# Optimization experiments

Hardware: AMD Instinct MI355X
Metric: run time of the kernel (lower is better)

The kernel has to match this reference:

```python
import jax, jax.numpy as jnp
import numpy as np

NUM_EXPERTS = 8
TOP_K = 2


def setup_inputs() -> dict:
    key = jax.random.key(0)
    ks = jax.random.split(key, 6)
    d, h, E = 512, 2048, NUM_EXPERTS
    s = 0.02
    return {
        "x": jax.random.normal(ks[0], (4, 4096, d), dtype=jnp.float32),
        "Wr": jax.random.normal(ks[1], (d, E), dtype=jnp.float32) * s,
        "W1": jax.random.normal(ks[2], (E, d, h), dtype=jnp.float32) * s,
        "b1": jax.random.normal(ks[3], (E, h), dtype=jnp.float32) * s,
        "W2": jax.random.normal(ks[4], (E, h, d), dtype=jnp.float32) * s,
        "b2": jax.random.normal(ks[5], (E, d), dtype=jnp.float32) * s,
    }


def reference(x, Wr, W1, b1, W2, b2):
    B, S, D = x.shape
    E = Wr.shape[1]
    flat = x.reshape(B * S, D)                      # [N, D]
    logits = flat @ Wr                              # [N, E]
    top_vals, top_idx = jax.lax.top_k(logits, TOP_K)  # [N, K]
    top_w = jax.nn.softmax(top_vals, axis=-1)       # [N, K]
    N = flat.shape[0]
    # dense gate matrix: weight per (token, expert); zero for unselected experts
    gates = jnp.zeros((N, E), dtype=flat.dtype).at[
        jnp.arange(N)[:, None], top_idx
    ].add(top_w)                                    # [N, E]
    out = jnp.zeros_like(flat)
    for e in range(E):  # small fixed expert count
        hdn = jax.nn.gelu(flat @ W1[e] + b1[e], approximate=False)  # [N, H]
        y = hdn @ W2[e] + b2[e]                                     # [N, D]
        out = out + gates[:, e:e + 1] * y
    return out.reshape(B, S, D)
```

## Files before the change

kernel.cpp:

```cpp
#include <hip/hip_runtime.h>
#include <math.h>

#define D_DIM 512
#define H_DIM 2048
#define NEXP  8

typedef __bf16 bf16x8 __attribute__((ext_vector_type(8)));
typedef float  f32x4  __attribute__((ext_vector_type(4)));

__device__ __forceinline__ unsigned short f2b(float f) {
    unsigned int u = __float_as_uint(f);
    unsigned int r = (u + 0x7FFFu + ((u >> 16) & 1u)) >> 16;
    return (unsigned short)r;
}

__device__ __forceinline__ float gelu_f(float v) {
    float z = fabsf(v) * 0.70710678118654752440f;
    float t = __builtin_amdgcn_rcpf(fmaf(0.3275911f, z, 1.0f));
    float poly = t * (0.254829592f +
                 t * (-0.284496736f +
                 t * (1.421413741f +
                 t * (-1.453152027f +
                 t * 1.061405429f))));
    float er = 1.0f - poly * __expf(-z * z);
    er = (v < 0.0f) ? -er : er;
    return 0.5f * v * (1.0f + er);
}

__device__ __forceinline__ void async_cp16(const void* g, void* l) {
    __builtin_amdgcn_global_load_lds(
        (const __attribute__((address_space(1))) unsigned int*)g,
        (__attribute__((address_space(3))) unsigned int*)l, 16, 0, 0);
}

__global__ void convert_x_kernel(const float* __restrict__ in,
                                 unsigned short* __restrict__ out, int n8) {
    int i = blockIdx.x * blockDim.x + threadIdx.x;
    if (i >= n8) return;
    const float4* p = (const float4*)(in + (size_t)i * 8);
    float4 a = p[0], b = p[1];
    unsigned short r[8] = {f2b(a.x), f2b(a.y), f2b(a.z), f2b(a.w),
                           f2b(b.x), f2b(b.y), f2b(b.z), f2b(b.w)};
    *(uint4*)(out + (size_t)i * 8) = *(const uint4*)r;
}

__global__ void transpose_conv_kernel(const float* __restrict__ in,
                                      unsigned short* __restrict__ out,
                                      int R, int C) {
    __shared__ unsigned short tile[64][72];
    int e = blockIdx.z;
    const float* ine = in + (size_t)e * R * C;
    unsigned short* oute = out + (size_t)e * C * R;
    int r0 = blockIdx.y * 64, c0 = blockIdx.x * 64;
    int tid = threadIdx.x;
#pragma unroll
    for (int rd = 0; rd < 4; ++rd) {
        int r = (tid >> 4) + rd * 16;
        int c = (tid & 15) * 4;
        float4 v = *(const float4*)&ine[(size_t)(r0 + r) * C + c0 + c];
        tile[c + 0][r] = f2b(v.x);
        tile[c + 1][r] = f2b(v.y);
        tile[c + 2][r] = f2b(v.z);
        tile[c + 3][r] = f2b(v.w);
    }
    __syncthreads();
    int cc = tid >> 2, rc = (tid & 3) * 16;
    unsigned short* op = oute + (size_t)(c0 + cc) * R + r0 + rc;
    *(uint4*)(op)     = *(const uint4*)&tile[cc][rc];
    *(uint4*)(op + 8) = *(const uint4*)&tile[cc][rc + 8];
}

__global__ void router_kernel(const float* __restrict__ x,
                              const float* __restrict__ Wr,
                              float* __restrict__ gate_w,
                              int* __restrict__ route,
                              int ntok) {
    int wid  = (blockIdx.x * blockDim.x + threadIdx.x) >> 6;
    int lane = threadIdx.x & 63;
    if (wid >= ntok) return;
    const float* xr = x + (size_t)wid * D_DIM;
    float acc[NEXP];
#pragma unroll
    for (int e = 0; e < NEXP; ++e) acc[e] = 0.0f;
#pragma unroll
    for (int it = 0; it < D_DIM / 64; ++it) {
        int d = it * 64 + lane;
        float xv = xr[d];
        const float* wr = Wr + d * NEXP;
#pragma unroll
        for (int e = 0; e < NEXP; ++e) acc[e] = fmaf(xv, wr[e], acc[e]);
    }
#pragma unroll
    for (int off = 32; off >= 1; off >>= 1) {
#pragma unroll
        for (int e = 0; e < NEXP; ++e) acc[e] += __shfl_xor(acc[e], off);
    }
    if (lane == 0) {
        int i0 = 0;
#pragma unroll
        for (int e = 1; e < NEXP; ++e) if (acc[e] > acc[i0]) i0 = e;
        int i1 = (i0 == 0) ? 1 : 0;
#pragma unroll
        for (int e = 0; e < NEXP; ++e) {
            if (e != i0 && acc[e] > acc[i1]) i1 = e;
        }
        float v0 = acc[i0], v1 = acc[i1];
        float ee = expf(v1 - v0);
        float inv = 1.0f / (1.0f + ee);
        int t = wid;
        gate_w[2 * t]     = inv;
        gate_w[2 * t + 1] = ee * inv;
        route[t] = i0 | (i1 << 8);
    }
}

__global__ void lists_kernel(const int* __restrict__ route,
                             int* __restrict__ lists,
                             int* __restrict__ cb,
                             int ntok) {
    __shared__ int wave_off[4];
    int e = blockIdx.x;
    int tid = threadIdx.x;
    int lane = tid & 63, w = tid >> 6;
    int running = 0;
    for (int c0 = 0; c0 < ntok; c0 += 256) {
        int t = c0 + tid;
        int rt = (t < ntok) ? route[t] : -1;
        int e0 = rt & 255, e1 = (rt >> 8) & 255;
        bool p1 = (e1 == e) && (rt >= 0);
        bool p  = ((e0 == e) && (rt >= 0)) || p1;
        unsigned long long mask = __ballot(p);
        int mypos = __popcll(mask & ((1ull << lane) - 1ull));
        int wcnt  = __popcll(mask);
        if (lane == 0) wave_off[w] = wcnt;
        __syncthreads();
        int wbase = 0;
#pragma unroll
        for (int i = 0; i < 4; ++i) if (i < w) wbase += wave_off[i];
        int total = wave_off[0] + wave_off[1] + wave_off[2] + wave_off[3];
        if (p) lists[(size_t)e * ntok + running + wbase + mypos] = 2 * t + (p1 ? 1 : 0);
        running += total;
        __syncthreads();
    }
    if (tid == 0) cb[e] = running;
}

__global__ void prefix_kernel(int* cb) {
    if (threadIdx.x == 0 && blockIdx.x == 0) {
        int s = 0;
#pragma unroll
        for (int e = 0; e < NEXP; ++e) { cb[8 + e] = s; s += cb[e]; }
    }
}

__global__ void bias_gate_kernel(const int* __restrict__ route,
                                 const float* __restrict__ gate_w,
                                 const float* __restrict__ b2,
                                 float* __restrict__ out, int ntok) {
    int t = blockIdx.x * 4 + (threadIdx.x >> 6);
    int lane = threadIdx.x & 63;
    if (t >= ntok) return;
    int rt = route[t];
    int e0 = rt & 255, e1 = (rt >> 8) & 255;
    float w0 = gate_w[2 * t], w1 = gate_w[2 * t + 1];
    const float4* p0 = (const float4*)(b2 + (size_t)e0 * D_DIM);
    const float4* p1 = (const float4*)(b2 + (size_t)e1 * D_DIM);
    float4* po = (float4*)(out + (size_t)t * D_DIM);
#pragma unroll
    for (int j = 0; j < 2; ++j) {
        float4 a = p0[lane * 2 + j], b = p1[lane * 2 + j];
        float4 r;
        r.x = w0 * a.x + w1 * b.x;
        r.y = w0 * a.y + w1 * b.y;
        r.z = w0 * a.z + w1 * b.z;
        r.w = w0 * a.w + w1 * b.w;
        po[lane * 2 + j] = r;
    }
}


__global__ __launch_bounds__(256, 2) void gemm1_kernel(
        const unsigned short* __restrict__ xb,
        const unsigned short* __restrict__ W1T,
        const float* __restrict__ b1,
        const float* __restrict__ gate_w,
        const int* __restrict__ lists,
        const int* __restrict__ cb,
        unsigned short* __restrict__ hdn,
        int ntok) {
    int bid = blockIdx.x;
    int e = bid & 7;
    int rest = bid >> 3;
    int ntile = rest & 15;
    int mt = rest >> 4;
    int cnt = cb[e];
    if (mt * 128 >= cnt) return;
    int base = cb[8 + e];

    __shared__ unsigned short As[2][8192];
    __shared__ unsigned short Bs[2][8192];
    __shared__ int   toksS[128];
    __shared__ float twS[128];

    int tid = threadIdx.x;
    int l = tid & 63, w = tid >> 6;
    int wm = (w & 1) * 64, wn = (w >> 1) * 64;

    if (tid < 128) {
        int idx = mt * 128 + tid;
        int entry = (idx < cnt) ? lists[(size_t)e * ntok + idx] : -1;
        toksS[tid] = (entry >= 0) ? (entry >> 1) : 0;
        twS[tid]   = (entry >= 0) ? gate_w[entry] : 0.0f;
    }
    __syncthreads();

    const char* Aglob[4];
    const char* Bglob[4];
    {
        int swz = ((l & 7) ^ (l >> 3)) * 16;
        const char* W1e = (const char*)(W1T + (size_t)e * H_DIM * D_DIM);
#pragma unroll
        for (int c = 0; c < 4; ++c) {
            int row = (w * 4 + c) * 8 + (l >> 3);
            Aglob[c] = (const char*)xb + (size_t)toksS[row] * 1024 + swz;
            Bglob[c] = W1e + (size_t)(ntile * 128 + row) * 1024 + swz;
        }
    }

    f32x4 acc[4][4];
#pragma unroll
    for (int i = 0; i < 4; ++i)
#pragma unroll
        for (int j = 0; j < 4; ++j) acc[i][j] = (f32x4){0.f, 0.f, 0.f, 0.f};

#pragma unroll
    for (int c = 0; c < 4; ++c) {
        async_cp16(Aglob[c], (char*)&As[0][0] + (w * 4 + c) * 1024);
        async_cp16(Bglob[c], (char*)&Bs[0][0] + (w * 4 + c) * 1024);
    }
    __syncthreads();

    for (int kc = 0; kc < 8; ++kc) {
        int cur = kc & 1;
        if (kc + 1 < 8) {
            int ko = (kc + 1) * 128;
#pragma unroll
            for (int c = 0; c < 4; ++c) {
                async_cp16(Aglob[c] + ko, (char*)&As[cur ^ 1][0] + (w * 4 + c) * 1024);
                async_cp16(Bglob[c] + ko, (char*)&Bs[cur ^ 1][0] + (w * 4 + c) * 1024);
            }
        }
        const char* Ab = (const char*)&As[cur][0];
        const char* Bb = (const char*)&Bs[cur][0];
#pragma unroll
        for (int ks = 0; ks < 2; ++ks) {
            int g = ks * 4 + (l >> 4);
            bf16x8 av[4], bv[4];
#pragma unroll
            for (int mf = 0; mf < 4; ++mf) {
                int m = wm + mf * 16 + (l & 15);
                av[mf] = *(const bf16x8*)(Ab + m * 128 + ((g ^ (m & 7)) * 16));
            }
#pragma unroll
            for (int nf = 0; nf < 4; ++nf) {
                int n = wn + nf * 16 + (l & 15);
                bv[nf] = *(const bf16x8*)(Bb + n * 128 + ((g ^ (n & 7)) * 16));
            }
#pragma unroll
            for (int mf = 0; mf < 4; ++mf)
#pragma unroll
                for (int nf = 0; nf < 4; ++nf)
                    acc[mf][nf] = __builtin_amdgcn_mfma_f32_16x16x32_bf16(
                        av[mf], bv[nf], acc[mf][nf], 0, 0, 0);
        }
        __syncthreads();
    }

    float twr[4][4];
#pragma unroll
    for (int mf = 0; mf < 4; ++mf)
#pragma unroll
        for (int r = 0; r < 4; ++r)
            twr[mf][r] = twS[wm + mf * 16 + (l >> 4) * 4 + r];
    const float* b1e = b1 + (size_t)e * H_DIM + ntile * 128;
    float b1v[4];
#pragma unroll
    for (int nf = 0; nf < 4; ++nf)
        b1v[nf] = b1e[wn + nf * 16 + (l & 15)];

    char* Lo = (char*)&As[0][0];
#pragma unroll
    for (int mf = 0; mf < 4; ++mf) {
#pragma unroll
        for (int nf = 0; nf < 4; ++nf) {
#pragma unroll
            for (int r = 0; r < 4; ++r) {
                int row = wm + mf * 16 + (l >> 4) * 4 + r;
                int col = wn + nf * 16 + (l & 15);
                float hv = twr[mf][r] * gelu_f(acc[mf][nf][r] + b1v[nf]);
                int byte = row * 256 + ((col * 2) ^ (((row >> 2) & 3) << 5));
                *(unsigned short*)(Lo + byte) = f2b(hv);
            }
        }
    }
    __syncthreads();
#pragma unroll
    for (int j = 0; j < 8; ++j) {
        int row = j * 16 + (tid >> 4);
        int c16 = tid & 15;
        uint4 v = *(const uint4*)(Lo + row * 256 + c16 * 16);
        int colchunk = c16 ^ (((row >> 2) & 3) << 1);
        int gr = mt * 128 + row;
        if (gr < cnt)
            *(uint4*)(hdn + (size_t)(base + gr) * H_DIM + ntile * 128 + colchunk * 8) = v;
    }
}

__global__ __launch_bounds__(256, 2) void gemm2_kernel(
        const unsigned short* __restrict__ hdn,
        const unsigned short* __restrict__ W2T,
        const int* __restrict__ lists,
        const int* __restrict__ cb,
        float* __restrict__ out,
        int ntok) {
    int bid = blockIdx.x;
    int e = bid & 7;
    int rest = bid >> 3;
    int ntile = rest & 3;
    int mt = rest >> 2;
    int cnt = cb[e];
    if (mt * 128 >= cnt) return;
    int base = cb[8 + e];

    __shared__ unsigned short As[2][8192];
    __shared__ unsigned short Bs[2][8192];
    __shared__ int toksS[128];

    int tid = threadIdx.x;
    int l = tid & 63, w = tid >> 6;
    int wm = (w & 1) * 64, wn = (w >> 1) * 64;

    if (tid < 128) {
        int idx = mt * 128 + tid;
        int entry = (idx < cnt) ? lists[(size_t)e * ntok + idx] : -1;
        toksS[tid] = (entry >= 0) ? (entry >> 1) : 0;
    }
    __syncthreads();

    const char* Aglob[4];
    const char* Bglob[4];
    {
        int swz = ((l & 7) ^ (l >> 3)) * 16;
        const char* W2e = (const char*)(W2T + (size_t)e * D_DIM * H_DIM);
#pragma unroll
        for (int c = 0; c < 4; ++c) {
            int row = (w * 4 + c) * 8 + (l >> 3);
            Aglob[c] = (const char*)hdn + (size_t)(base + mt * 128 + row) * 4096 + swz;
            Bglob[c] = W2e + (size_t)(ntile * 128 + row) * 4096 + swz;
        }
    }

    f32x4 acc[4][4];
#pragma unroll
    for (int i = 0; i < 4; ++i)
#pragma unroll
        for (int j = 0; j < 4; ++j) acc[i][j] = (f32x4){0.f, 0.f, 0.f, 0.f};

#pragma unroll
    for (int c = 0; c < 4; ++c) {
        async_cp16(Aglob[c], (char*)&As[0][0] + (w * 4 + c) * 1024);
        async_cp16(Bglob[c], (char*)&Bs[0][0] + (w * 4 + c) * 1024);
    }
    __syncthreads();

    for (int kc = 0; kc < 32; ++kc) {
        int cur = kc & 1;
        if (kc + 1 < 32) {
            int ko = (kc + 1) * 128;
#pragma unroll
            for (int c = 0; c < 4; ++c) {
                async_cp16(Aglob[c] + ko, (char*)&As[cur ^ 1][0] + (w * 4 + c) * 1024);
                async_cp16(Bglob[c] + ko, (char*)&Bs[cur ^ 1][0] + (w * 4 + c) * 1024);
            }
        }
        const char* Ab = (const char*)&As[cur][0];
        const char* Bb = (const char*)&Bs[cur][0];
#pragma unroll
        for (int ks = 0; ks < 2; ++ks) {
            int g = ks * 4 + (l >> 4);
            bf16x8 av[4], bv[4];
#pragma unroll
            for (int mf = 0; mf < 4; ++mf) {
                int m = wm + mf * 16 + (l & 15);
                av[mf] = *(const bf16x8*)(Ab + m * 128 + ((g ^ (m & 7)) * 16));
            }
#pragma unroll
            for (int nf = 0; nf < 4; ++nf) {
                int n = wn + nf * 16 + (l & 15);
                bv[nf] = *(const bf16x8*)(Bb + n * 128 + ((g ^ (n & 7)) * 16));
            }
#pragma unroll
            for (int mf = 0; mf < 4; ++mf)
#pragma unroll
                for (int nf = 0; nf < 4; ++nf)
                    acc[mf][nf] = __builtin_amdgcn_mfma_f32_16x16x32_bf16(
                        av[mf], bv[nf], acc[mf][nf], 0, 0, 0);
        }
        __syncthreads();
    }

#pragma unroll
    for (int mf = 0; mf < 4; ++mf) {
#pragma unroll
        for (int r = 0; r < 4; ++r) {
            int rl = wm + mf * 16 + (l >> 4) * 4 + r;
            int gr = mt * 128 + rl;
            if (gr < cnt) {
                float* op = out + (size_t)toksS[rl] * D_DIM + ntile * 128 + wn;
#pragma unroll
                for (int nf = 0; nf < 4; ++nf)
                    atomicAdd(op + nf * 16 + (l & 15), acc[mf][nf][r]);
            }
        }
    }
}

#define FBT 64
#define FKC 64
#define FHC 64
#define FTPB 512

__global__ __launch_bounds__(FTPB) void moe_fused_fallback(
        const float* __restrict__ x,
        const float* __restrict__ W1, const float* __restrict__ b1,
        const float* __restrict__ W2, const float* __restrict__ b2,
        const float* __restrict__ gate_w,
        const int* __restrict__ lists, const int* __restrict__ counts,
        float* __restrict__ out, int ntok, int tiles) {
    __shared__ __align__(16) float ldsA[FBT][FKC + 4];
    __shared__ __align__(16) float ldsB[FKC][FHC + 4];
    __shared__ int   toks[FBT];
    __shared__ float tw[FBT];
    int e = blockIdx.x / tiles;
    int tile = blockIdx.x % tiles;
    int cnt = counts[e];
    if (tile * FBT >= cnt) return;
    int tid = threadIdx.x;
    int srow = tid >> 3, scol = (tid & 7) * 8;
    int tg2 = tid >> 4, sg4 = tid & 15;
    if (tid < FBT) {
        int idx = tile * FBT + tid;
        int entry = (idx < cnt) ? lists[(size_t)e * ntok + idx] : -1;
        toks[tid] = (entry >= 0) ? (entry >> 1) : 0;
        tw[tid]   = (entry >= 0) ? gate_w[entry] : 0.0f;
    }
    __syncthreads();
    float yacc[2][32];
#pragma unroll
    for (int p = 0; p < 2; ++p)
#pragma unroll
        for (int i = 0; i < 32; ++i) yacc[p][i] = 0.0f;
    const float* W1e = W1 + (size_t)e * D_DIM * H_DIM;
    const float* W2e = W2 + (size_t)e * H_DIM * D_DIM;
    const float* b1e = b1 + (size_t)e * H_DIM;
    int t0 = tg2, t1 = tg2 + 32;
    for (int hc = 0; hc < H_DIM / FHC; ++hc) {
        float pre[2][4];
#pragma unroll
        for (int p = 0; p < 2; ++p)
#pragma unroll
            for (int j = 0; j < 4; ++j) pre[p][j] = 0.0f;
        for (int kc = 0; kc < D_DIM / FKC; ++kc) {
            __syncthreads();
            {
                const float* src = x + (size_t)toks[srow] * D_DIM + kc * FKC + scol;
                *(float4*)&ldsA[srow][scol]     = *(const float4*)(src);
                *(float4*)&ldsA[srow][scol + 4] = *(const float4*)(src + 4);
                const float* ws1 = W1e + (size_t)(kc * FKC + srow) * H_DIM + hc * FHC + scol;
                *(float4*)&ldsB[srow][scol]     = *(const float4*)(ws1);
                *(float4*)&ldsB[srow][scol + 4] = *(const float4*)(ws1 + 4);
            }
            __syncthreads();
#pragma unroll
            for (int k = 0; k < FKC; ++k) {
                float a0 = ldsA[t0][k], a1 = ldsA[t1][k];
                const float4 b4 = *(const float4*)&ldsB[k][sg4 * 4];
                pre[0][0] = fmaf(a0, b4.x, pre[0][0]);
                pre[0][1] = fmaf(a0, b4.y, pre[0][1]);
                pre[0][2] = fmaf(a0, b4.z, pre[0][2]);
                pre[0][3] = fmaf(a0, b4.w, pre[0][3]);
                pre[1][0] = fmaf(a1, b4.x, pre[1][0]);
                pre[1][1] = fmaf(a1, b4.y, pre[1][1]);
                pre[1][2] = fmaf(a1, b4.z, pre[1][2]);
                pre[1][3] = fmaf(a1, b4.w, pre[1][3]);
            }
        }
        __syncthreads();
        {
            const float* b1p = b1e + hc * FHC + sg4 * 4;
            float4 h0, h1;
            h0.x = gelu_f(pre[0][0] + b1p[0]); h0.y = gelu_f(pre[0][1] + b1p[1]);
            h0.z = gelu_f(pre[0][2] + b1p[2]); h0.w = gelu_f(pre[0][3] + b1p[3]);
            h1.x = gelu_f(pre[1][0] + b1p[0]); h1.y = gelu_f(pre[1][1] + b1p[1]);
            h1.z = gelu_f(pre[1][2] + b1p[2]); h1.w = gelu_f(pre[1][3] + b1p[3]);
            *(float4*)&ldsA[t0][sg4 * 4] = h0;
            *(float4*)&ldsA[t1][sg4 * 4] = h1;
        }
        for (int dt = 0; dt < 8; ++dt) {
            __syncthreads();
            {
                const float* ws2 = W2e + (size_t)(hc * FHC + srow) * D_DIM + dt * 64 + scol;
                *(float4*)&ldsB[srow][scol]     = *(const float4*)(ws2);
                *(float4*)&ldsB[srow][scol + 4] = *(const float4*)(ws2 + 4);
            }
            __syncthreads();
#pragma unroll
            for (int hh = 0; hh < FHC; ++hh) {
                float a0 = ldsA[t0][hh], a1 = ldsA[t1][hh];
                const float4 b4 = *(const float4*)&ldsB[hh][sg4 * 4];
                yacc[0][dt * 4 + 0] = fmaf(a0, b4.x, yacc[0][dt * 4 + 0]);
                yacc[0][dt * 4 + 1] = fmaf(a0, b4.y, yacc[0][dt * 4 + 1]);
                yacc[0][dt * 4 + 2] = fmaf(a0, b4.z, yacc[0][dt * 4 + 2]);
                yacc[0][dt * 4 + 3] = fmaf(a0, b4.w, yacc[0][dt * 4 + 3]);
                yacc[1][dt * 4 + 0] = fmaf(a1, b4.x, yacc[1][dt * 4 + 0]);
                yacc[1][dt * 4 + 1] = fmaf(a1, b4.y, yacc[1][dt * 4 + 1]);
                yacc[1][dt * 4 + 2] = fmaf(a1, b4.z, yacc[1][dt * 4 + 2]);
                yacc[1][dt * 4 + 3] = fmaf(a1, b4.w, yacc[1][dt * 4 + 3]);
            }
        }
    }
    const float* b2e = b2 + (size_t)e * D_DIM;
#pragma unroll
    for (int p = 0; p < 2; ++p) {
        int slot = (p == 0) ? t0 : t1;
        if (tile * FBT + slot < cnt) {
            float wv = tw[slot];
            float* op = out + (size_t)toks[slot] * D_DIM;
#pragma unroll
            for (int dt = 0; dt < 8; ++dt)
#pragma unroll
                for (int j = 0; j < 4; ++j) {
                    int d = dt * 64 + sg4 * 4 + j;
                    atomicAdd(&op[d], wv * (yacc[p][dt * 4 + j] + b2e[d]));
                }
        }
    }
}

extern "C" void kernel_launch(void* const* d_in, const int* in_sizes, int n_in,
                              void* d_out, int out_size, void* d_ws, size_t ws_size,
                              hipStream_t stream) {
    const float* x  = (const float*)d_in[0];
    const float* Wr = (const float*)d_in[1];
    const float* W1 = (const float*)d_in[2];
    const float* b1 = (const float*)d_in[3];
    const float* W2 = (const float*)d_in[4];
    const float* b2 = (const float*)d_in[5];
    float* out = (float*)d_out;
    int ntok = in_sizes[0] / D_DIM;

    size_t off_route = 256;
    size_t off_gate  = off_route + (size_t)ntok * 4;
    size_t off_lists = off_gate + (size_t)2 * ntok * 4;
    size_t off_xb    = off_lists + (size_t)NEXP * ntok * 4;
    size_t off_w1t   = off_xb + (size_t)ntok * D_DIM * 2;
    size_t off_w2t   = off_w1t + (size_t)NEXP * D_DIM * H_DIM * 2;
    size_t off_hdn   = off_w2t + (size_t)NEXP * D_DIM * H_DIM * 2;
    size_t need      = off_hdn + (size_t)(2 * ntok + 128) * H_DIM * 2;

    int*   cb     = (int*)d_ws;
    int*   route  = (int*)((char*)d_ws + off_route);
    float* gate_w = (float*)((char*)d_ws + off_gate);
    int*   lists  = (int*)((char*)d_ws + off_lists);

    if (ws_size >= need) {
        unsigned short* xb  = (unsigned short*)((char*)d_ws + off_xb);
        unsigned short* W1T = (unsigned short*)((char*)d_ws + off_w1t);
        unsigned short* W2T = (unsigned short*)((char*)d_ws + off_w2t);
        unsigned short* hdn = (unsigned short*)((char*)d_ws + off_hdn);

        int n8 = ntok * D_DIM / 8;
        convert_x_kernel<<<(n8 + 255) / 256, 256, 0, stream>>>(x, xb, n8);
        transpose_conv_kernel<<<dim3(H_DIM / 64, D_DIM / 64, NEXP), 256, 0, stream>>>(
            W1, W1T, D_DIM, H_DIM);
        transpose_conv_kernel<<<dim3(D_DIM / 64, H_DIM / 64, NEXP), 256, 0, stream>>>(
            W2, W2T, H_DIM, D_DIM);
        router_kernel<<<(ntok + 3) / 4, 256, 0, stream>>>(
            x, Wr, gate_w, route, ntok);
        lists_kernel<<<NEXP, 256, 0, stream>>>(route, lists, cb, ntok);
        prefix_kernel<<<1, 64, 0, stream>>>(cb);
        bias_gate_kernel<<<(ntok + 3) / 4, 256, 0, stream>>>(
            route, gate_w, b2, out, ntok);
        int mtiles = ntok / 128;
        gemm1_kernel<<<NEXP * 16 * mtiles, 256, 0, stream>>>(
            xb, W1T, b1, gate_w, lists, cb, hdn, ntok);
        gemm2_kernel<<<NEXP * 4 * mtiles, 256, 0, stream>>>(
            hdn, W2T, lists, cb, out, ntok);
    } else {
        hipMemsetAsync(d_out, 0, (size_t)out_size * sizeof(float), stream);
        router_kernel<<<(ntok + 3) / 4, 256, 0, stream>>>(
            x, Wr, gate_w, route, ntok);
        lists_kernel<<<NEXP, 256, 0, stream>>>(route, lists, cb, ntok);
        prefix_kernel<<<1, 64, 0, stream>>>(cb);
        int tiles = (ntok + FBT - 1) / FBT;
        moe_fused_fallback<<<NEXP * tiles, FTPB, 0, stream>>>(
            x, W1, b1, W2, b2, gate_w, lists, cb, out, ntok, tiles);
    }
}
```

Baseline: 359.9 us.

## Single-buffer GEMM LDS for higher occupancy; fuse x bf16 conversion into router

```diff
diff --git a/kernel.cpp b/kernel.cpp
--- a/kernel.cpp
+++ b/kernel.cpp
@@ -33,17 +33,6 @@
         (__attribute__((address_space(3))) unsigned int*)l, 16, 0, 0);
 }
 
-__global__ void convert_x_kernel(const float* __restrict__ in,
-                                 unsigned short* __restrict__ out, int n8) {
-    int i = blockIdx.x * blockDim.x + threadIdx.x;
-    if (i >= n8) return;
-    const float4* p = (const float4*)(in + (size_t)i * 8);
-    float4 a = p[0], b = p[1];
-    unsigned short r[8] = {f2b(a.x), f2b(a.y), f2b(a.z), f2b(a.w),
-                           f2b(b.x), f2b(b.y), f2b(b.z), f2b(b.w)};
-    *(uint4*)(out + (size_t)i * 8) = *(const uint4*)r;
-}
-
 __global__ void transpose_conv_kernel(const float* __restrict__ in,
                                       unsigned short* __restrict__ out,
                                       int R, int C) {
@@ -74,6 +63,7 @@
                               const float* __restrict__ Wr,
                               float* __restrict__ gate_w,
                               int* __restrict__ route,
+                              unsigned short* __restrict__ xbout,
                               int ntok) {
     int wid  = (blockIdx.x * blockDim.x + threadIdx.x) >> 6;
     int lane = threadIdx.x & 63;
@@ -86,6 +76,7 @@
     for (int it = 0; it < D_DIM / 64; ++it) {
         int d = it * 64 + lane;
         float xv = xr[d];
+        if (xbout) xbout[(size_t)wid * D_DIM + d] = f2b(xv);
         const float* wr = Wr + d * NEXP;
 #pragma unroll
         for (int e = 0; e < NEXP; ++e) acc[e] = fmaf(xv, wr[e], acc[e]);
@@ -179,7 +170,7 @@
 }
 
 
-__global__ __launch_bounds__(256, 2) void gemm1_kernel(
+__global__ __launch_bounds__(256, 4) void gemm1_kernel(
         const unsigned short* __restrict__ xb,
         const unsigned short* __restrict__ W1T,
         const float* __restrict__ b1,
@@ -197,10 +188,11 @@
     if (mt * 128 >= cnt) return;
     int base = cb[8 + e];
 
-    __shared__ unsigned short As[2][8192];
-    __shared__ unsigned short Bs[2][8192];
+    __shared__ unsigned short AsBs[16384];
     __shared__ int   toksS[128];
     __shared__ float twS[128];
+    unsigned short* As = AsBs;
+    unsigned short* Bs = AsBs + 8192;
 
     int tid = threadIdx.x;
     int l = tid & 63, w = tid >> 6;
@@ -233,25 +225,15 @@
 #pragma unroll
         for (int j = 0; j < 4; ++j) acc[i][j] = (f32x4){0.f, 0.f, 0.f, 0.f};
 
-#pragma unroll
-    for (int c = 0; c < 4; ++c) {
-        async_cp16(Aglob[c], (char*)&As[0][0] + (w * 4 + c) * 1024);
-        async_cp16(Bglob[c], (char*)&Bs[0][0] + (w * 4 + c) * 1024);
-    }
-    __syncthreads();
-
     for (int kc = 0; kc < 8; ++kc) {
-        int cur = kc & 1;
-        if (kc + 1 < 8) {
-            int ko = (kc + 1) * 128;
-#pragma unroll
-            for (int c = 0; c < 4; ++c) {
-                async_cp16(Aglob[c] + ko, (char*)&As[cur ^ 1][0] + (w * 4 + c) * 1024);
-                async_cp16(Bglob[c] + ko, (char*)&Bs[cur ^ 1][0] + (w * 4 + c) * 1024);
-            }
-        }
-        const char* Ab = (const char*)&As[cur][0];
-        const char* Bb = (const char*)&Bs[cur][0];
+        __syncthreads();
+        int ko = kc * 128;
+#pragma unroll
+        for (int c = 0; c < 4; ++c) {
+            async_cp16(Aglob[c] + ko, (char*)As + (w * 4 + c) * 1024);
+            async_cp16(Bglob[c] + ko, (char*)Bs + (w * 4 + c) * 1024);
+        }
+        __syncthreads();
 #pragma unroll
         for (int ks = 0; ks < 2; ++ks) {
             int g = ks * 4 + (l >> 4);
@@ -259,12 +241,12 @@
 #pragma unroll
             for (int mf = 0; mf < 4; ++mf) {
                 int m = wm + mf * 16 + (l & 15);
-                av[mf] = *(const bf16x8*)(Ab + m * 128 + ((g ^ (m & 7)) * 16));
+                av[mf] = *(const bf16x8*)((const char*)As + m * 128 + ((g ^ (m & 7)) * 16));
             }
 #pragma unroll
             for (int nf = 0; nf < 4; ++nf) {
                 int n = wn + nf * 16 + (l & 15);
-                bv[nf] = *(const bf16x8*)(Bb + n * 128 + ((g ^ (n & 7)) * 16));
+                bv[nf] = *(const bf16x8*)((const char*)Bs + n * 128 + ((g ^ (n & 7)) * 16));
             }
 #pragma unroll
             for (int mf = 0; mf < 4; ++mf)
@@ -273,7 +255,6 @@
                     acc[mf][nf] = __builtin_amdgcn_mfma_f32_16x16x32_bf16(
                         av[mf], bv[nf], acc[mf][nf], 0, 0, 0);
         }
-        __syncthreads();
     }
 
     float twr[4][4];
@@ -288,7 +269,8 @@
     for (int nf = 0; nf < 4; ++nf)
         b1v[nf] = b1e[wn + nf * 16 + (l & 15)];
 
-    char* Lo = (char*)&As[0][0];
+    __syncthreads();
+    char* Lo = (char*)AsBs;
 #pragma unroll
     for (int mf = 0; mf < 4; ++mf) {
 #pragma unroll
@@ -316,7 +298,7 @@
     }
 }
 
-__global__ __launch_bounds__(256, 2) void gemm2_kernel(
+__global__ __launch_bounds__(256, 4) void gemm2_kernel(
         const unsigned short* __restrict__ hdn,
         const unsigned short* __restrict__ W2T,
         const int* __restrict__ lists,
@@ -332,9 +314,10 @@
     if (mt * 128 >= cnt) return;
     int base = cb[8 + e];
 
-    __shared__ unsigned short As[2][8192];
-    __shared__ unsigned short Bs[2][8192];
+    __shared__ unsigned short AsBs[16384];
     __shared__ int toksS[128];
+    unsigned short* As = AsBs;
+    unsigned short* Bs = AsBs + 8192;
 
     int tid = threadIdx.x;
     int l = tid & 63, w = tid >> 6;
@@ -366,25 +349,15 @@
 #pragma unroll
         for (int j = 0; j < 4; ++j) acc[i][j] = (f32x4){0.f, 0.f, 0.f, 0.f};
 
-#pragma unroll
-    for (int c = 0; c < 4; ++c) {
-        async_cp16(Aglob[c], (char*)&As[0][0] + (w * 4 + c) * 1024);
-        async_cp16(Bglob[c], (char*)&Bs[0][0] + (w * 4 + c) * 1024);
-    }
-    __syncthreads();
-
     for (int kc = 0; kc < 32; ++kc) {
-        int cur = kc & 1;
-        if (kc + 1 < 32) {
-            int ko = (kc + 1) * 128;
-#pragma unroll
-            for (int c = 0; c < 4; ++c) {
-                async_cp16(Aglob[c] + ko, (char*)&As[cur ^ 1][0] + (w * 4 + c) * 1024);
-                async_cp16(Bglob[c] + ko, (char*)&Bs[cur ^ 1][0] + (w * 4 + c) * 1024);
-            }
-        }
-        const char* Ab = (const char*)&As[cur][0];
-        const char* Bb = (const char*)&Bs[cur][0];
+        __syncthreads();
+        int ko = kc * 128;
+#pragma unroll
+        for (int c = 0; c < 4; ++c) {
+            async_cp16(Aglob[c] + ko, (char*)As + (w * 4 + c) * 1024);
+            async_cp16(Bglob[c] + ko, (char*)Bs + (w * 4 + c) * 1024);
+        }
+        __syncthreads();
 #pragma unroll
         for (int ks = 0; ks < 2; ++ks) {
             int g = ks * 4 + (l >> 4);
@@ -392,12 +365,12 @@
 #pragma unroll
             for (int mf = 0; mf < 4; ++mf) {
                 int m = wm + mf * 16 + (l & 15);
-                av[mf] = *(const bf16x8*)(Ab + m * 128 + ((g ^ (m & 7)) * 16));
+                av[mf] = *(const bf16x8*)((const char*)As + m * 128 + ((g ^ (m & 7)) * 16));
             }
 #pragma unroll
             for (int nf = 0; nf < 4; ++nf) {
                 int n = wn + nf * 16 + (l & 15);
-                bv[nf] = *(const bf16x8*)(Bb + n * 128 + ((g ^ (n & 7)) * 16));
+                bv[nf] = *(const bf16x8*)((const char*)Bs + n * 128 + ((g ^ (n & 7)) * 16));
             }
 #pragma unroll
             for (int mf = 0; mf < 4; ++mf)
@@ -406,7 +379,6 @@
                     acc[mf][nf] = __builtin_amdgcn_mfma_f32_16x16x32_bf16(
                         av[mf], bv[nf], acc[mf][nf], 0, 0, 0);
         }
-        __syncthreads();
     }
 
 #pragma unroll
@@ -579,14 +551,12 @@
         unsigned short* W2T = (unsigned short*)((char*)d_ws + off_w2t);
         unsigned short* hdn = (unsigned short*)((char*)d_ws + off_hdn);
 
-        int n8 = ntok * D_DIM / 8;
-        convert_x_kernel<<<(n8 + 255) / 256, 256, 0, stream>>>(x, xb, n8);
         transpose_conv_kernel<<<dim3(H_DIM / 64, D_DIM / 64, NEXP), 256, 0, stream>>>(
             W1, W1T, D_DIM, H_DIM);
         transpose_conv_kernel<<<dim3(D_DIM / 64, H_DIM / 64, NEXP), 256, 0, stream>>>(
             W2, W2T, H_DIM, D_DIM);
         router_kernel<<<(ntok + 3) / 4, 256, 0, stream>>>(
-            x, Wr, gate_w, route, ntok);
+            x, Wr, gate_w, route, xb, ntok);
         lists_kernel<<<NEXP, 256, 0, stream>>>(route, lists, cb, ntok);
         prefix_kernel<<<1, 64, 0, stream>>>(cb);
         bias_gate_kernel<<<(ntok + 3) / 4, 256, 0, stream>>>(
@@ -599,7 +569,7 @@
     } else {
         hipMemsetAsync(d_out, 0, (size_t)out_size * sizeof(float), stream);
         router_kernel<<<(ntok + 3) / 4, 256, 0, stream>>>(
-            x, Wr, gate_w, route, ntok);
+            x, Wr, gate_w, route, (unsigned short*)0, ntok);
         lists_kernel<<<NEXP, 256, 0, stream>>>(route, lists, cb, ntok);
         prefix_kernel<<<1, 64, 0, stream>>>(cb);
         int tiles = (ntok + FBT - 1) / FBT;
```

Result: faster. 315.7 us (-12.3%).
